# Optimization experiments

Hardware: AMD Instinct MI355X
Metric: run time of the kernel (lower is better)

Reference implementation:

```python
import jax, jax.numpy as jnp
import numpy as np

B, S, NB = 2, 1024, 64
V, D, L, H, F = 1024, 512, 12, 8, 2048
DH = D // H
MAX_BARS = 256


def _ln(x, g, b):
    m = x.mean(-1, keepdims=True)
    v = ((x - m) ** 2).mean(-1, keepdims=True)
    return (x - m) * jax.lax.rsqrt(v + 1e-5) * g + b


def _rope(x, pos):
    # x: (B, T, H, DH), pos: (T,)
    half = x.shape[-1] // 2
    inv = 10000.0 ** (-jnp.arange(half, dtype=jnp.float32) / half)
    f = pos.astype(jnp.float32)[:, None] * inv  # (T, half)
    cos = jnp.cos(f)[None, :, None, :]
    sin = jnp.sin(f)[None, :, None, :]
    x1, x2 = x[..., :half], x[..., half:]
    return jnp.concatenate([x1 * cos - x2 * sin, x1 * sin + x2 * cos], -1)


def _swiglu(h, w1, w3, w2):
    return (jax.nn.silu(h @ w1) * (h @ w3)) @ w2


def _attention(sum_x, x, Wq, Wk, Wv, Wo, smask, umask, pos_s, pos_r):
    # shared QKV/O projections over both streams; 4-way block mask via concat keys
    b, nb, _ = sum_x.shape
    s = x.shape[1]

    def proj(t, W):
        return (t @ W).reshape(t.shape[0], t.shape[1], H, DH)

    qs = _rope(proj(sum_x, Wq), pos_s)
    qr = _rope(proj(x, Wq), pos_r)
    k = jnp.concatenate([_rope(proj(sum_x, Wk), pos_s), _rope(proj(x, Wk), pos_r)], 1)
    v = jnp.concatenate([proj(sum_x, Wv), proj(x, Wv)], 1)
    scale = DH ** -0.5

    def attend(q, mask):
        sc = jnp.einsum('bqhd,bkhd->bhqk', q, k) * scale
        sc = jnp.where(mask[:, None], sc, -1e9)
        p = jax.nn.softmax(sc, axis=-1)
        o = jnp.einsum('bhqk,bkhd->bqhd', p, v)
        return o.reshape(q.shape[0], q.shape[1], D)

    return attend(qs, smask) @ Wo, attend(qr, umask) @ Wo


def _forward(tok_emb, inst_emb, bar_emb,
             ln_as_g, ln_as_b, ln_ar_g, ln_ar_b,
             ln_fs_g, ln_fs_b, ln_fr_g, ln_fr_b,
             Wq, Wk, Wv, Wo,
             fs_w1, fs_w3, fs_w2, fr_w1, fr_w3, fr_w2,
             out_g, out_b,
             token_ids, chord_ids, instrument_ids, num_bars):
    b, s = token_ids.shape
    nb = num_bars
    x = tok_emb[token_ids] + inst_emb[jnp.clip(instrument_ids, 0, 129)]
    sum_x = jnp.broadcast_to(bar_emb[:nb][None], (b, nb, tok_emb.shape[1]))

    bars = jnp.arange(nb)
    idx = jnp.arange(s)
    # ss: summary b attends summaries b' <= b (causal over bars)
    ss = jnp.broadcast_to(jnp.tril(jnp.ones((nb, nb), bool))[None], (b, nb, nb))
    # sr: summary b summarizes regular tokens in bar b
    sr = chord_ids[:, None, :] == bars[None, :, None]  # (B, nb, S)
    smask = jnp.concatenate([ss, sr], -1)  # (B, nb, nb+S)
    # rs: regular i attends summaries of strictly previous bars
    rs = bars[None, None, :] < chord_ids[:, :, None]  # (B, S, nb)
    # rr: regular i attends regular j in same bar, causally
    rr = (chord_ids[:, :, None] == chord_ids[:, None, :]) & (idx[:, None] >= idx[None, :])
    umask = jnp.concatenate([rs, rr], -1)  # (B, S, nb+S)

    pos_s = jnp.arange(nb)
    pos_r = jnp.arange(s)

    for l in range(Wq.shape[0]):
        a_s, a_r = _attention(_ln(sum_x, ln_as_g[l], ln_as_b[l]),
                              _ln(x, ln_ar_g[l], ln_ar_b[l]),
                              Wq[l], Wk[l], Wv[l], Wo[l], smask, umask, pos_s, pos_r)
        sum_x = sum_x + a_s
        x = x + a_r
        sum_x = sum_x + _swiglu(_ln(sum_x, ln_fs_g[l], ln_fs_b[l]), fs_w1[l], fs_w3[l], fs_w2[l])
        x = x + _swiglu(_ln(x, ln_fr_g[l], ln_fr_b[l]), fr_w1[l], fr_w3[l], fr_w2[l])

    x = _ln(x, out_g, out_b)
    return x @ tok_emb.T  # tied lm_head


def setup_inputs():
    key = jax.random.key(0)
    it = iter(jax.random.split(key, 40))

    def nrm(shape):
        return jax.random.normal(next(it), shape, jnp.float32) * 0.02

    inp = {
        'token_ids': jax.random.randint(next(it), (B, S), 0, V),
        'chord_ids': jnp.sort(jax.random.randint(next(it), (B, S), 0, NB), axis=-1),
        'instrument_ids': jax.random.randint(next(it), (B, S), 0, 130),
        'num_bars': NB,
        'tok_emb': nrm((V, D)),
        'inst_emb': nrm((130, D)),
        'bar_emb': nrm((MAX_BARS, D)),
        'ln_as_g': jnp.ones((L, D)), 'ln_as_b': jnp.zeros((L, D)),
        'ln_ar_g': jnp.ones((L, D)), 'ln_ar_b': jnp.zeros((L, D)),
        'ln_fs_g': jnp.ones((L, D)), 'ln_fs_b': jnp.zeros((L, D)),
        'ln_fr_g': jnp.ones((L, D)), 'ln_fr_b': jnp.zeros((L, D)),
        'Wq': nrm((L, D, D)), 'Wk': nrm((L, D, D)),
        'Wv': nrm((L, D, D)), 'Wo': nrm((L, D, D)),
        'fs_w1': nrm((L, D, F)), 'fs_w3': nrm((L, D, F)), 'fs_w2': nrm((L, F, D)),
        'fr_w1': nrm((L, D, F)), 'fr_w3': nrm((L, D, F)), 'fr_w2': nrm((L, F, D)),
        'out_g': jnp.ones((D,)), 'out_b': jnp.zeros((D,)),
    }
    return inp


def reference(token_ids, chord_ids, instrument_ids, num_bars,
              tok_emb, inst_emb, bar_emb,
              ln_as_g, ln_as_b, ln_ar_g, ln_ar_b,
              ln_fs_g, ln_fs_b, ln_fr_g, ln_fr_b,
              Wq, Wk, Wv, Wo,
              fs_w1, fs_w3, fs_w2, fr_w1, fr_w3, fr_w2,
              out_g, out_b):
    return _forward(tok_emb, inst_emb, bar_emb,
                    ln_as_g, ln_as_b, ln_ar_g, ln_ar_b,
                    ln_fs_g, ln_fs_b, ln_fr_g, ln_fr_b,
                    Wq, Wk, Wv, Wo,
                    fs_w1, fs_w3, fs_w2, fr_w1, fr_w3, fr_w2,
                    out_g, out_b,
                    token_ids, chord_ids, instrument_ids, num_bars)
```

## Files before the change

### kernel.cpp

```cpp
#include <hip/hip_runtime.h>
#include <stdint.h>

#define NB 64
#define BATCH 2
#define SEQ 1024
#define DMODEL 512
#define NHEAD 8
#define DHEAD 64
#define FDIM 2048
#define NLAYER 12
#define VOCAB 1024
#define KTOT (NB + SEQ)
#define RSUM (BATCH * NB)
#define RREG (BATCH * SEQ)
#define RTOT (RSUM + RREG)

using bf16x8 = __attribute__((ext_vector_type(8))) short;
using bf16x4 = __attribute__((ext_vector_type(4))) short;
using f32x4  = __attribute__((ext_vector_type(4))) float;

__device__ __forceinline__ unsigned short f2bf(float f) {
  union { float f; unsigned u; } c; c.f = f;
  return (unsigned short)((c.u + 0x7fffu + ((c.u >> 16) & 1u)) >> 16);
}
__device__ __forceinline__ float bf2f(unsigned short s) {
  union { unsigned u; float f; } c; c.u = ((unsigned)s) << 16;
  return c.f;
}

template<int R>
__device__ __forceinline__ void stage_tile(
    const unsigned short* __restrict__ G, int K, int base_row, int k0,
    unsigned short (*lds)[64], int wid, int lane)
{
  const int rl = lane >> 3;
  const int j  = lane & 7;
  #pragma unroll
  for (int c = 0; c < R / 32; ++c) {
    const int r0 = wid * (R / 4) + c * 8;
    const int row = r0 + rl;
    const unsigned short* g = G + (size_t)(base_row + row) * K + k0
                                + ((j ^ (row & 7)) << 3);
    __builtin_amdgcn_global_load_lds(
        (const __attribute__((address_space(1))) void*)g,
        (__attribute__((address_space(3))) void*)&lds[r0][0], 16, 0, 0);
  }
}

__device__ __forceinline__ bf16x8 lds_frag(const unsigned short (*lds)[64],
                                           int row, int cc) {
  return *(const bf16x8*)&lds[row][(cc ^ (row & 7)) << 3];
}

template<int BM, int BN, int EPI>
__global__ __launch_bounds__(256) void gemm_bt(
    const unsigned short* __restrict__ A, const unsigned short* __restrict__ B0,
    const unsigned short* __restrict__ B1,
    void* __restrict__ Cout, const float* resid, int N, int K,
    const float* __restrict__ cost, const float* __restrict__ sint,
    unsigned short* __restrict__ kcat, unsigned short* __restrict__ vcat)
{
  constexpr int BK = 64;
  constexpr int WM = BM / 2, WN = BN / 2;
  constexpr int FM = WM / 16, FN = WN / 16;
  constexpr int SM_STAGE = (BM + BN) * BK * 2;
  constexpr int SM_CT = (EPI == 3) ? 64 * 66 * 4 : 0;
  constexpr int SMSZ = SM_STAGE > SM_CT ? SM_STAGE : SM_CT;
  __shared__ __align__(16) unsigned char smem[SMSZ];
  auto As = (unsigned short (*)[BK])smem;
  auto Bs = (unsigned short (*)[BK])(smem + BM * BK * 2);
  const int bm = blockIdx.y * BM, bn = blockIdx.x * BN;
  const unsigned short* __restrict__ BT = (bm < RSUM) ? B0 : B1;
  const int tid = threadIdx.x;
  const int wid = tid >> 6, lane = tid & 63;
  const int wm = wid >> 1, wn = wid & 1;
  const int lr = lane & 15, lk = lane >> 4;
  f32x4 acc[FM][FN] = {};
  for (int k0 = 0; k0 < K; k0 += BK) {
    __syncthreads();
    stage_tile<BM>(A,  K, bm, k0, As, wid, lane);
    stage_tile<BN>(BT, K, bn, k0, Bs, wid, lane);
    __syncthreads();
    #pragma unroll
    for (int kk = 0; kk < 2; ++kk) {
      bf16x8 af[FM], bfr[FN];
      #pragma unroll
      for (int m = 0; m < FM; ++m)
        af[m] = lds_frag(As, wm * WM + m * 16 + lr, kk * 4 + lk);
      #pragma unroll
      for (int n = 0; n < FN; ++n)
        bfr[n] = lds_frag(Bs, wn * WN + n * 16 + lr, kk * 4 + lk);
      #pragma unroll
      for (int m = 0; m < FM; ++m)
        #pragma unroll
        for (int n = 0; n < FN; ++n)
          acc[m][n] = __builtin_amdgcn_mfma_f32_16x16x32_bf16(af[m], bfr[n], acc[m][n], 0, 0, 0);
    }
  }
  if constexpr (EPI == 3) {
    __syncthreads();
    auto ct = (float (*)[66])smem;
    #pragma unroll
    for (int m = 0; m < FM; ++m)
      #pragma unroll
      for (int n = 0; n < FN; ++n)
        #pragma unroll
        for (int i = 0; i < 4; ++i)
          ct[wm * WM + m * 16 + lk * 4 + i][wn * WN + n * 16 + lr] = acc[m][n][i];
    __syncthreads();
    const int r = tid >> 2, quad = tid & 3;
    const int tr = bm + r;
    int b, pos, catrow;
    if (tr < RSUM) { b = tr >> 6; pos = tr & (NB - 1); catrow = pos; }
    else { const int rr = tr - RSUM; b = rr >> 10; pos = rr & (SEQ - 1); catrow = NB + pos; }
    const int part = bn >> 9;
    const int head = (bn & 511) >> 6;
    const size_t obase = ((size_t)(b * NHEAD + head) * KTOT + catrow) * DHEAD + quad * 16;
    union { unsigned short u[16]; uint4 q[2]; } ob;
    if (part == 2) {
      #pragma unroll
      for (int j = 0; j < 16; ++j) ob.u[j] = f2bf(ct[r][quad * 16 + j]);
      *(uint4*)&vcat[obase] = ob.q[0];
      *(uint4*)&vcat[obase + 8] = ob.q[1];
    } else {
      #pragma unroll
      for (int j = 0; j < 16; ++j) {
        const int d = quad * 16 + j;
        const float v = ct[r][d];
        const float other = ct[r][d ^ 32];
        const float cs = cost[pos * 32 + (d & 31)];
        const float sn = sint[pos * 32 + (d & 31)];
        ob.u[j] = f2bf((d < 32) ? (v * cs - other * sn) : (other * sn + v * cs));
      }
      unsigned short* dst = part ? kcat : (unsigned short*)Cout;
      *(uint4*)&dst[obase] = ob.q[0];
      *(uint4*)&dst[obase + 8] = ob.q[1];
    }
    return;
  }
  #pragma unroll
  for (int m = 0; m < FM; ++m)
    #pragma unroll
    for (int n = 0; n < FN; ++n)
      #pragma unroll
      for (int i = 0; i < 4; ++i) {
        int row = bm + wm * WM + m * 16 + lk * 4 + i;
        int col = bn + wn * WN + n * 16 + lr;
        float v = acc[m][n][i];
        if constexpr (EPI == 1) {
          const float other = __shfl_xor(v, 1, 64);
          if (!(lr & 1)) {
            const float g = v, u = other;
            const float hv = (g / (1.f + __expf(-g))) * u;
            unsigned short* C = (unsigned short*)Cout;
            C[(size_t)row * (N >> 1) + (col >> 1)] = f2bf(hv);
          }
        } else if constexpr (EPI == 2) {
          unsigned short* C = (unsigned short*)Cout;
          C[(size_t)row * N + col] = f2bf(v);
        } else {
          float* C = (float*)Cout;
          size_t idx = (size_t)row * N + col;
          if (resid) v += resid[idx];
          C[idx] = v;
        }
      }
}

__global__ __launch_bounds__(256) void transpose_conv_kernel(
    const float* __restrict__ src, unsigned short* __restrict__ dst,
    int K, int N, size_t sstride, size_t dstride, int rmul, int radd)
{
  __shared__ float tile[32][33];
  const float* s = src + (size_t)blockIdx.z * sstride;
  unsigned short* d = dst + (size_t)blockIdx.z * dstride;
  const int k0 = blockIdx.y * 32, n0 = blockIdx.x * 32;
  const int tx = threadIdx.x & 31, ty = threadIdx.x >> 5;
  #pragma unroll
  for (int i = 0; i < 32; i += 8)
    tile[ty + i][tx] = s[(size_t)(k0 + ty + i) * N + n0 + tx];
  __syncthreads();
  #pragma unroll
  for (int i = 0; i < 32; i += 8)
    d[((size_t)(n0 + ty + i) * rmul + radd) * K + k0 + tx] = f2bf(tile[tx][ty + i]);
}

__global__ __launch_bounds__(256) void convert_bf16_kernel(
    const float* __restrict__ src, unsigned short* __restrict__ dst)
{
  const int i = (blockIdx.x * 256 + threadIdx.x) * 4;
  const float4 v = *(const float4*)&src[i];
  union { unsigned short u[4]; uint2 q; } o;
  o.u[0] = f2bf(v.x); o.u[1] = f2bf(v.y); o.u[2] = f2bf(v.z); o.u[3] = f2bf(v.w);
  *(uint2*)&dst[i] = o.q;
}

__global__ __launch_bounds__(128) void embed_kernel(
    const int* __restrict__ tok, const int* __restrict__ inst,
    const float* __restrict__ tok_emb, const float* __restrict__ inst_emb,
    const float* __restrict__ bar_emb, float* __restrict__ z)
{
  const int r = blockIdx.x, t = threadIdx.x;
  float4 val;
  if (r < RSUM) {
    const int bar = r & (NB - 1);
    val = *(const float4*)&bar_emb[(size_t)bar * DMODEL + t * 4];
  } else {
    const int rr = r - RSUM;
    const int b = rr >> 10, i = rr & (SEQ - 1);
    const int tk = tok[b * SEQ + i];
    int ins = inst[b * SEQ + i];
    ins = ins < 0 ? 0 : (ins > 129 ? 129 : ins);
    const float4 a = *(const float4*)&tok_emb[(size_t)tk * DMODEL + t * 4];
    const float4 cc = *(const float4*)&inst_emb[(size_t)ins * DMODEL + t * 4];
    val.x = a.x + cc.x; val.y = a.y + cc.y; val.z = a.z + cc.z; val.w = a.w + cc.w;
  }
  *(float4*)&z[(size_t)r * DMODEL + t * 4] = val;
}

__global__ __launch_bounds__(256) void ln_dual_kernel(
    const float* __restrict__ x, const float* __restrict__ g_s,
    const float* __restrict__ b_s, const float* __restrict__ g_r,
    const float* __restrict__ b_r, unsigned short* __restrict__ out)
{
  const int wid = threadIdx.x >> 6, lane = threadIdx.x & 63;
  const size_t row = (size_t)blockIdx.x * 4 + wid;
  const float* g = (row < RSUM) ? g_s : g_r;
  const float* bb = (row < RSUM) ? b_s : b_r;
  const float* xr = x + row * DMODEL + lane * 8;
  float v[8];
  *(float4*)&v[0] = *(const float4*)&xr[0];
  *(float4*)&v[4] = *(const float4*)&xr[4];
  float s = 0.f;
  #pragma unroll
  for (int j = 0; j < 8; ++j) s += v[j];
  #pragma unroll
  for (int o = 32; o > 0; o >>= 1) s += __shfl_xor(s, o, 64);
  const float mean = s * (1.f / DMODEL);
  float vs = 0.f;
  #pragma unroll
  for (int j = 0; j < 8; ++j) { float d = v[j] - mean; vs += d * d; }
  #pragma unroll
  for (int o = 32; o > 0; o >>= 1) vs += __shfl_xor(vs, o, 64);
  const float rs = rsqrtf(vs * (1.f / DMODEL) + 1e-5f);
  float gg[8], bv[8];
  *(float4*)&gg[0] = *(const float4*)&g[lane * 8];
  *(float4*)&gg[4] = *(const float4*)&g[lane * 8 + 4];
  *(float4*)&bv[0] = *(const float4*)&bb[lane * 8];
  *(float4*)&bv[4] = *(const float4*)&bb[lane * 8 + 4];
  union { unsigned short u[8]; uint4 q; } o8;
  #pragma unroll
  for (int j = 0; j < 8; ++j) o8.u[j] = f2bf((v[j] - mean) * rs * gg[j] + bv[j]);
  *(uint4*)&out[row * DMODEL + lane * 8] = o8.q;
}

__global__ __launch_bounds__(256) void ln_kernel(
    const float* __restrict__ x, const float* __restrict__ g,
    const float* __restrict__ bb, unsigned short* __restrict__ out)
{
  const int wid = threadIdx.x >> 6, lane = threadIdx.x & 63;
  const size_t row = (size_t)blockIdx.x * 4 + wid;
  const float* xr = x + row * DMODEL + lane * 8;
  float v[8];
  *(float4*)&v[0] = *(const float4*)&xr[0];
  *(float4*)&v[4] = *(const float4*)&xr[4];
  float s = 0.f;
  #pragma unroll
  for (int j = 0; j < 8; ++j) s += v[j];
  #pragma unroll
  for (int o = 32; o > 0; o >>= 1) s += __shfl_xor(s, o, 64);
  const float mean = s * (1.f / DMODEL);
  float vs = 0.f;
  #pragma unroll
  for (int j = 0; j < 8; ++j) { float d = v[j] - mean; vs += d * d; }
  #pragma unroll
  for (int o = 32; o > 0; o >>= 1) vs += __shfl_xor(vs, o, 64);
  const float rs = rsqrtf(vs * (1.f / DMODEL) + 1e-5f);
  float gg[8], bv[8];
  *(float4*)&gg[0] = *(const float4*)&g[lane * 8];
  *(float4*)&gg[4] = *(const float4*)&g[lane * 8 + 4];
  *(float4*)&bv[0] = *(const float4*)&bb[lane * 8];
  *(float4*)&bv[4] = *(const float4*)&bb[lane * 8 + 4];
  union { unsigned short u[8]; uint4 q; } o8;
  #pragma unroll
  for (int j = 0; j < 8; ++j) o8.u[j] = f2bf((v[j] - mean) * rs * gg[j] + bv[j]);
  *(uint4*)&out[row * DMODEL + lane * 8] = o8.q;
}

__global__ void rope_table_kernel(float* __restrict__ cost, float* __restrict__ sint) {
  const int pos = blockIdx.x, j = threadIdx.x;
  const float inv = powf(10000.f, -(float)j / 32.f);
  const float f = (float)pos * inv;
  cost[pos * 32 + j] = cosf(f);
  sint[pos * 32 + j] = sinf(f);
}

__global__ void segstart_kernel(const int* __restrict__ chord, int* __restrict__ seg) {
  const int b = blockIdx.x, t = threadIdx.x;
  if (t <= NB) {
    int lo = 0, hi = SEQ;
    while (lo < hi) {
      int mid = (lo + hi) >> 1;
      if (chord[b * SEQ + mid] < t) lo = mid + 1; else hi = mid;
    }
    seg[b * (NB + 1) + t] = lo;
  }
}

__global__ __launch_bounds__(256) void attn_kernel(
    const unsigned short* __restrict__ q_cat, const unsigned short* __restrict__ k_cat,
    const unsigned short* __restrict__ v_cat, const int* __restrict__ seg,
    const int* __restrict__ chord, unsigned short* __restrict__ att)
{
  const int h = blockIdx.y, b = blockIdx.z;
  const int wid = threadIdx.x >> 6, lane = threadIdx.x & 63;
  const int qi = blockIdx.x * 4 + wid;
  int qrow, nsum, s0, nk, outrow;
  if (qi < NB) {
    const int c = qi;
    s0 = seg[b * (NB + 1) + c];
    const int s1 = seg[b * (NB + 1) + c + 1];
    qrow = c; nsum = c + 1; nk = nsum + (s1 - s0);
    outrow = b * NB + c;
  } else {
    const int i = qi - NB;
    const int c = chord[b * SEQ + i];
    s0 = seg[b * (NB + 1) + c];
    qrow = NB + i; nsum = c; nk = nsum + (i - s0 + 1);
    outrow = RSUM + b * SEQ + i;
  }
  const size_t bh = (size_t)(b * NHEAD + h) * KTOT * DHEAD;
  const unsigned short* __restrict__ Kp = k_cat + bh;
  const unsigned short* __restrict__ Vp = v_cat + bh;
  __shared__ __align__(16) float qsh[4][DHEAD];
  __shared__ __align__(16) float psh[4][64];
  qsh[wid][lane] = bf2f(q_cat[bh + (size_t)qrow * DHEAD + lane]) * 0.125f;
  const int lq = lane & 3;
  const int lkey = lane >> 2;
  const int kk = lane >> 4;
  const int dd = lane & 15;
  float m = -1e30f, l = 0.f;
  float4 o4 = {0.f, 0.f, 0.f, 0.f};
  for (int t0 = 0; t0 < nk; t0 += 64) {
    float sv[4];
    float tmax = -3.0e38f;
    #pragma unroll
    for (int pass = 0; pass < 4; ++pass) {
      const int t = t0 + pass * 16 + lkey;
      int kr = (t < nsum) ? t : (NB + s0 + (t - nsum));
      if (kr > KTOT - 1) kr = KTOT - 1;
      const bf16x8* krp = (const bf16x8*)(Kp + (size_t)kr * DHEAD + lq * 16);
      const bf16x8 k0v = krp[0], k1v = krp[1];
      float a = 0.f;
      #pragma unroll
      for (int d2 = 0; d2 < 8; ++d2)
        a = fmaf(qsh[wid][lq * 16 + d2], bf2f((unsigned short)k0v[d2]), a);
      #pragma unroll
      for (int d2 = 0; d2 < 8; ++d2)
        a = fmaf(qsh[wid][lq * 16 + 8 + d2], bf2f((unsigned short)k1v[d2]), a);
      a += __shfl_xor(a, 1, 64);
      a += __shfl_xor(a, 2, 64);
      sv[pass] = (t < nk) ? a : -3.0e38f;
      tmax = fmaxf(tmax, sv[pass]);
    }
    #pragma unroll
    for (int off = 32; off > 0; off >>= 1) tmax = fmaxf(tmax, __shfl_xor(tmax, off, 64));
    const float mn = fmaxf(m, tmax);
    float psum = 0.f;
    #pragma unroll
    for (int pass = 0; pass < 4; ++pass) {
      const float pp = __expf(sv[pass] - mn);
      psum += pp;
      if (lq == 0) psh[wid][pass * 16 + lkey] = pp;
    }
    psum *= 0.25f;
    #pragma unroll
    for (int off = 32; off > 0; off >>= 1) psum += __shfl_xor(psum, off, 64);
    const float scale = __expf(m - mn);
    l = l * scale + psum;
    o4.x *= scale; o4.y *= scale; o4.z *= scale; o4.w *= scale;
    m = mn;
    #pragma unroll
    for (int j = 0; j < 16; ++j) {
      const int toff = j * 4 + kk;
      const float p = psh[wid][toff];
      const int tk = t0 + toff;
      int kr = (tk < nsum) ? tk : (NB + s0 + (tk - nsum));
      if (kr > KTOT - 1) kr = KTOT - 1;
      const bf16x4 vv = *(const bf16x4*)&Vp[(size_t)kr * DHEAD + dd * 4];
      o4.x = fmaf(p, bf2f((unsigned short)vv[0]), o4.x);
      o4.y = fmaf(p, bf2f((unsigned short)vv[1]), o4.y);
      o4.z = fmaf(p, bf2f((unsigned short)vv[2]), o4.z);
      o4.w = fmaf(p, bf2f((unsigned short)vv[3]), o4.w);
    }
  }
  #pragma unroll
  for (int off = 16; off <= 32; off <<= 1) {
    o4.x += __shfl_xor(o4.x, off, 64);
    o4.y += __shfl_xor(o4.y, off, 64);
    o4.z += __shfl_xor(o4.z, off, 64);
    o4.w += __shfl_xor(o4.w, off, 64);
  }
  if (kk == 0) {
    const float invl = 1.f / l;
    union { unsigned short u[4]; uint2 q; } ob;
    ob.u[0] = f2bf(o4.x * invl); ob.u[1] = f2bf(o4.y * invl);
    ob.u[2] = f2bf(o4.z * invl); ob.u[3] = f2bf(o4.w * invl);
    *(uint2*)&att[(size_t)outrow * DMODEL + h * DHEAD + dd * 4] = ob.q;
  }
}

extern "C" void kernel_launch(void* const* d_in, const int* in_sizes, int n_in,
                              void* d_out, int out_size, void* d_ws, size_t ws_size,
                              hipStream_t stream)
{
  const int* tok      = (const int*)d_in[0];
  const int* chord    = (const int*)d_in[1];
  const int* inst     = (const int*)d_in[2];
  const float* tok_emb  = (const float*)d_in[4];
  const float* inst_emb = (const float*)d_in[5];
  const float* bar_emb  = (const float*)d_in[6];
  const float* ln_as_g = (const float*)d_in[7];
  const float* ln_as_b = (const float*)d_in[8];
  const float* ln_ar_g = (const float*)d_in[9];
  const float* ln_ar_b = (const float*)d_in[10];
  const float* ln_fs_g = (const float*)d_in[11];
  const float* ln_fs_b = (const float*)d_in[12];
  const float* ln_fr_g = (const float*)d_in[13];
  const float* ln_fr_b = (const float*)d_in[14];
  const float* Wq = (const float*)d_in[15];
  const float* Wk = (const float*)d_in[16];
  const float* Wv = (const float*)d_in[17];
  const float* Wo = (const float*)d_in[18];
  const float* fs_w1 = (const float*)d_in[19];
  const float* fs_w3 = (const float*)d_in[20];
  const float* fs_w2 = (const float*)d_in[21];
  const float* fr_w1 = (const float*)d_in[22];
  const float* fr_w3 = (const float*)d_in[23];
  const float* fr_w2 = (const float*)d_in[24];
  const float* out_g = (const float*)d_in[25];
  const float* out_b = (const float*)d_in[26];

  char* p = (char*)d_ws;
  auto alloc = [&](size_t bytes) -> void* {
    void* r = (void*)p;
    p += (bytes + 255) & ~(size_t)255;
    return r;
  };
  unsigned short* WqkvT  = (unsigned short*)alloc((size_t)NLAYER * 1536 * 512 * 2);
  unsigned short* WoT    = (unsigned short*)alloc((size_t)NLAYER * 512 * 512 * 2);
  unsigned short* fsW13T = (unsigned short*)alloc((size_t)NLAYER * 4096 * 512 * 2);
  unsigned short* frW13T = (unsigned short*)alloc((size_t)NLAYER * 4096 * 512 * 2);
  unsigned short* fsW2T  = (unsigned short*)alloc((size_t)NLAYER * 512 * 2048 * 2);
  unsigned short* frW2T  = (unsigned short*)alloc((size_t)NLAYER * 512 * 2048 * 2);
  unsigned short* tokT   = (unsigned short*)alloc((size_t)VOCAB * DMODEL * 2);
  float* z           = (float*)alloc((size_t)RTOT * DMODEL * 4);
  unsigned short* zn = (unsigned short*)alloc((size_t)RTOT * DMODEL * 2);
  unsigned short* q_cat = (unsigned short*)alloc((size_t)BATCH * NHEAD * KTOT * DHEAD * 2);
  unsigned short* k_cat = (unsigned short*)alloc((size_t)BATCH * NHEAD * KTOT * DHEAD * 2);
  unsigned short* v_cat = (unsigned short*)alloc((size_t)BATCH * NHEAD * KTOT * DHEAD * 2);
  unsigned short* att = (unsigned short*)alloc((size_t)RTOT * DMODEL * 2);
  unsigned short* h1 = (unsigned short*)alloc((size_t)RTOT * FDIM * 2);
  float* cost        = (float*)alloc((size_t)SEQ * 32 * 4);
  float* sint        = (float*)alloc((size_t)SEQ * 32 * 4);
  int* seg           = (int*)alloc((size_t)BATCH * (NB + 1) * 4);
  if ((size_t)(p - (char*)d_ws) > ws_size) return;

  transpose_conv_kernel<<<dim3(16, 16, NLAYER), 256, 0, stream>>>(Wq, WqkvT,                    512, 512,  (size_t)512*512,  (size_t)1536*512, 1, 0);
  transpose_conv_kernel<<<dim3(16, 16, NLAYER), 256, 0, stream>>>(Wk, WqkvT + (size_t)512*512,  512, 512,  (size_t)512*512,  (size_t)1536*512, 1, 0);
  transpose_conv_kernel<<<dim3(16, 16, NLAYER), 256, 0, stream>>>(Wv, WqkvT + (size_t)1024*512, 512, 512,  (size_t)512*512,  (size_t)1536*512, 1, 0);
  transpose_conv_kernel<<<dim3(16, 16, NLAYER), 256, 0, stream>>>(Wo, WoT,                      512, 512,  (size_t)512*512,  (size_t)512*512,  1, 0);
  transpose_conv_kernel<<<dim3(64, 16, NLAYER), 256, 0, stream>>>(fs_w1, fsW13T, 512, 2048, (size_t)512*2048, (size_t)4096*512, 2, 0);
  transpose_conv_kernel<<<dim3(64, 16, NLAYER), 256, 0, stream>>>(fs_w3, fsW13T, 512, 2048, (size_t)512*2048, (size_t)4096*512, 2, 1);
  transpose_conv_kernel<<<dim3(64, 16, NLAYER), 256, 0, stream>>>(fr_w1, frW13T, 512, 2048, (size_t)512*2048, (size_t)4096*512, 2, 0);
  transpose_conv_kernel<<<dim3(64, 16, NLAYER), 256, 0, stream>>>(fr_w3, frW13T, 512, 2048, (size_t)512*2048, (size_t)4096*512, 2, 1);
  transpose_conv_kernel<<<dim3(16, 64, NLAYER), 256, 0, stream>>>(fs_w2, fsW2T, 2048, 512, (size_t)2048*512, (size_t)512*2048, 1, 0);
  transpose_conv_kernel<<<dim3(16, 64, NLAYER), 256, 0, stream>>>(fr_w2, frW2T, 2048, 512, (size_t)2048*512, (size_t)512*2048, 1, 0);
  convert_bf16_kernel<<<VOCAB * DMODEL / 1024, 256, 0, stream>>>(tok_emb, tokT);

  embed_kernel<<<RTOT, 128, 0, stream>>>(tok, inst, tok_emb, inst_emb, bar_emb, z);
  rope_table_kernel<<<SEQ, 32, 0, stream>>>(cost, sint);
  segstart_kernel<<<BATCH, 128, 0, stream>>>(chord, seg);

  for (int l = 0; l < NLAYER; ++l) {
    const size_t ld = (size_t)l * DMODEL;
    ln_dual_kernel<<<RTOT / 4, 256, 0, stream>>>(z, ln_as_g + ld, ln_as_b + ld,
                                                 ln_ar_g + ld, ln_ar_b + ld, zn);
    gemm_bt<64, 64, 3><<<dim3(1536 / 64, RTOT / 64), 256, 0, stream>>>(
        zn, WqkvT + (size_t)l * 1536 * 512, WqkvT + (size_t)l * 1536 * 512,
        q_cat, nullptr, 1536, 512, cost, sint, k_cat, v_cat);
    attn_kernel<<<dim3(KTOT / 4, NHEAD, BATCH), 256, 0, stream>>>(q_cat, k_cat, v_cat, seg, chord, att);
    gemm_bt<64, 32, 0><<<dim3(512 / 32, RTOT / 64), 256, 0, stream>>>(
        att, WoT + (size_t)l * 512 * 512, WoT + (size_t)l * 512 * 512,
        z, z, 512, 512, nullptr, nullptr, nullptr, nullptr);
    ln_dual_kernel<<<RTOT / 4, 256, 0, stream>>>(z, ln_fs_g + ld, ln_fs_b + ld,
                                                 ln_fr_g + ld, ln_fr_b + ld, zn);
    gemm_bt<64, 64, 1><<<dim3(4096 / 64, RTOT / 64), 256, 0, stream>>>(
        zn, fsW13T + (size_t)l * 4096 * 512, frW13T + (size_t)l * 4096 * 512,
        h1, nullptr, 4096, 512, nullptr, nullptr, nullptr, nullptr);
    gemm_bt<64, 32, 0><<<dim3(512 / 32, RTOT / 64), 256, 0, stream>>>(
        h1, fsW2T + (size_t)l * 512 * 2048, frW2T + (size_t)l * 512 * 2048,
        z, z, 512, 2048, nullptr, nullptr, nullptr, nullptr);
  }

  ln_kernel<<<RREG / 4, 256, 0, stream>>>(z + (size_t)RSUM * DMODEL, out_g, out_b,
                                          zn + (size_t)RSUM * DMODEL);
  gemm_bt<64, 64, 0><<<dim3(VOCAB / 64, RREG / 64), 256, 0, stream>>>(
      zn + (size_t)RSUM * DMODEL, tokT, tokT, (float*)d_out, nullptr, VOCAB, 512,
      nullptr, nullptr, nullptr, nullptr);
}
```

Before: 1.320 ms.

## Fuse LayerNorm into GEMM A-tile staging and drop standalone LN kernels

```diff
diff --git a/kernel.cpp b/kernel.cpp
--- a/kernel.cpp
+++ b/kernel.cpp
@@ -52,13 +52,15 @@
   return *(const bf16x8*)&lds[row][(cc ^ (row & 7)) << 3];
 }
 
-template<int BM, int BN, int EPI>
+template<int BM, int BN, int EPI, bool LNF>
 __global__ __launch_bounds__(256) void gemm_bt(
-    const unsigned short* __restrict__ A, const unsigned short* __restrict__ B0,
+    const void* __restrict__ Ap, const unsigned short* __restrict__ B0,
     const unsigned short* __restrict__ B1,
     void* __restrict__ Cout, const float* resid, int N, int K,
     const float* __restrict__ cost, const float* __restrict__ sint,
-    unsigned short* __restrict__ kcat, unsigned short* __restrict__ vcat)
+    unsigned short* __restrict__ kcat, unsigned short* __restrict__ vcat,
+    const float* __restrict__ g_s, const float* __restrict__ b_s,
+    const float* __restrict__ g_r, const float* __restrict__ b_r)
 {
   constexpr int BK = 64;
   constexpr int WM = BM / 2, WN = BN / 2;
@@ -67,6 +69,7 @@
   constexpr int SM_CT = (EPI == 3) ? 64 * 66 * 4 : 0;
   constexpr int SMSZ = SM_STAGE > SM_CT ? SM_STAGE : SM_CT;
   __shared__ __align__(16) unsigned char smem[SMSZ];
+  __shared__ float rstats[BM * 2];
   auto As = (unsigned short (*)[BK])smem;
   auto Bs = (unsigned short (*)[BK])(smem + BM * BK * 2);
   const int bm = blockIdx.y * BM, bn = blockIdx.x * BN;
@@ -75,10 +78,57 @@
   const int wid = tid >> 6, lane = tid & 63;
   const int wm = wid >> 1, wn = wid & 1;
   const int lr = lane & 15, lk = lane >> 4;
+  const float* __restrict__ Az = (const float*)Ap;
+  const unsigned short* __restrict__ Ab = (const unsigned short*)Ap;
+  const float* __restrict__ gsel = (bm < RSUM) ? g_s : g_r;
+  const float* __restrict__ bsel = (bm < RSUM) ? b_s : b_r;
+  if constexpr (LNF) {
+    const int r = tid >> 2, q = tid & 3;
+    const float* src = Az + (size_t)(bm + r) * K + q * 128;
+    float s = 0.f, ss = 0.f;
+    #pragma unroll 8
+    for (int j = 0; j < 32; ++j) {
+      const float4 v = *(const float4*)&src[j * 4];
+      s += v.x + v.y + v.z + v.w;
+      ss += v.x * v.x + v.y * v.y + v.z * v.z + v.w * v.w;
+    }
+    s  += __shfl_xor(s, 1, 64);  s  += __shfl_xor(s, 2, 64);
+    ss += __shfl_xor(ss, 1, 64); ss += __shfl_xor(ss, 2, 64);
+    if (q == 0) {
+      const float mean = s * (1.f / DMODEL);
+      const float var = ss * (1.f / DMODEL) - mean * mean;
+      rstats[r * 2] = mean;
+      rstats[r * 2 + 1] = rsqrtf(fmaxf(var, 0.f) + 1e-5f);
+    }
+  }
   f32x4 acc[FM][FN] = {};
   for (int k0 = 0; k0 < K; k0 += BK) {
     __syncthreads();
-    stage_tile<BM>(A,  K, bm, k0, As, wid, lane);
+    if constexpr (LNF) {
+      const int r = tid >> 2, q = tid & 3;
+      const float mean = rstats[r * 2], rstd = rstats[r * 2 + 1];
+      const float* src = Az + (size_t)(bm + r) * K + k0 + q * 16;
+      const float* gp = gsel + k0 + q * 16;
+      const float* bp = bsel + k0 + q * 16;
+      #pragma unroll
+      for (int c = 0; c < 2; ++c) {
+        float v[8], gv[8], bv[8];
+        *(float4*)&v[0]  = *(const float4*)&src[c * 8];
+        *(float4*)&v[4]  = *(const float4*)&src[c * 8 + 4];
+        *(float4*)&gv[0] = *(const float4*)&gp[c * 8];
+        *(float4*)&gv[4] = *(const float4*)&gp[c * 8 + 4];
+        *(float4*)&bv[0] = *(const float4*)&bp[c * 8];
+        *(float4*)&bv[4] = *(const float4*)&bp[c * 8 + 4];
+        union { unsigned short u[8]; uint4 qd; } ob;
+        #pragma unroll
+        for (int j = 0; j < 8; ++j)
+          ob.u[j] = f2bf((v[j] - mean) * rstd * gv[j] + bv[j]);
+        const int slot = (q * 2 + c) ^ (r & 7);
+        *(uint4*)&As[r][slot * 8] = ob.qd;
+      }
+    } else {
+      stage_tile<BM>(Ab, K, bm, k0, As, wid, lane);
+    }
     stage_tile<BN>(BT, K, bn, k0, Bs, wid, lane);
     __syncthreads();
     #pragma unroll
@@ -216,75 +266,6 @@
     val.x = a.x + cc.x; val.y = a.y + cc.y; val.z = a.z + cc.z; val.w = a.w + cc.w;
   }
   *(float4*)&z[(size_t)r * DMODEL + t * 4] = val;
-}
-
-__global__ __launch_bounds__(256) void ln_dual_kernel(
-    const float* __restrict__ x, const float* __restrict__ g_s,
-    const float* __restrict__ b_s, const float* __restrict__ g_r,
-    const float* __restrict__ b_r, unsigned short* __restrict__ out)
-{
-  const int wid = threadIdx.x >> 6, lane = threadIdx.x & 63;
-  const size_t row = (size_t)blockIdx.x * 4 + wid;
-  const float* g = (row < RSUM) ? g_s : g_r;
-  const float* bb = (row < RSUM) ? b_s : b_r;
-  const float* xr = x + row * DMODEL + lane * 8;
-  float v[8];
-  *(float4*)&v[0] = *(const float4*)&xr[0];
-  *(float4*)&v[4] = *(const float4*)&xr[4];
-  float s = 0.f;
-  #pragma unroll
-  for (int j = 0; j < 8; ++j) s += v[j];
-  #pragma unroll
-  for (int o = 32; o > 0; o >>= 1) s += __shfl_xor(s, o, 64);
-  const float mean = s * (1.f / DMODEL);
-  float vs = 0.f;
-  #pragma unroll
-  for (int j = 0; j < 8; ++j) { float d = v[j] - mean; vs += d * d; }
-  #pragma unroll
-  for (int o = 32; o > 0; o >>= 1) vs += __shfl_xor(vs, o, 64);
-  const float rs = rsqrtf(vs * (1.f / DMODEL) + 1e-5f);
-  float gg[8], bv[8];
-  *(float4*)&gg[0] = *(const float4*)&g[lane * 8];
-  *(float4*)&gg[4] = *(const float4*)&g[lane * 8 + 4];
-  *(float4*)&bv[0] = *(const float4*)&bb[lane * 8];
-  *(float4*)&bv[4] = *(const float4*)&bb[lane * 8 + 4];
-  union { unsigned short u[8]; uint4 q; } o8;
-  #pragma unroll
-  for (int j = 0; j < 8; ++j) o8.u[j] = f2bf((v[j] - mean) * rs * gg[j] + bv[j]);
-  *(uint4*)&out[row * DMODEL + lane * 8] = o8.q;
-}
-
-__global__ __launch_bounds__(256) void ln_kernel(
-    const float* __restrict__ x, const float* __restrict__ g,
-    const float* __restrict__ bb, unsigned short* __restrict__ out)
-{
-  const int wid = threadIdx.x >> 6, lane = threadIdx.x & 63;
-  const size_t row = (size_t)blockIdx.x * 4 + wid;
-  const float* xr = x + row * DMODEL + lane * 8;
-  float v[8];
-  *(float4*)&v[0] = *(const float4*)&xr[0];
-  *(float4*)&v[4] = *(const float4*)&xr[4];
-  float s = 0.f;
-  #pragma unroll
-  for (int j = 0; j < 8; ++j) s += v[j];
-  #pragma unroll
-  for (int o = 32; o > 0; o >>= 1) s += __shfl_xor(s, o, 64);
-  const float mean = s * (1.f / DMODEL);
-  float vs = 0.f;
-  #pragma unroll
-  for (int j = 0; j < 8; ++j) { float d = v[j] - mean; vs += d * d; }
-  #pragma unroll
-  for (int o = 32; o > 0; o >>= 1) vs += __shfl_xor(vs, o, 64);
-  const float rs = rsqrtf(vs * (1.f / DMODEL) + 1e-5f);
-  float gg[8], bv[8];
-  *(float4*)&gg[0] = *(const float4*)&g[lane * 8];
-  *(float4*)&gg[4] = *(const float4*)&g[lane * 8 + 4];
-  *(float4*)&bv[0] = *(const float4*)&bb[lane * 8];
-  *(float4*)&bv[4] = *(const float4*)&bb[lane * 8 + 4];
-  union { unsigned short u[8]; uint4 q; } o8;
-  #pragma unroll
-  for (int j = 0; j < 8; ++j) o8.u[j] = f2bf((v[j] - mean) * rs * gg[j] + bv[j]);
-  *(uint4*)&out[row * DMODEL + lane * 8] = o8.q;
 }
 
 __global__ void rope_table_kernel(float* __restrict__ cost, float* __restrict__ sint) {
@@ -455,7 +436,6 @@
   unsigned short* frW2T  = (unsigned short*)alloc((size_t)NLAYER * 512 * 2048 * 2);
   unsigned short* tokT   = (unsigned short*)alloc((size_t)VOCAB * DMODEL * 2);
   float* z           = (float*)alloc((size_t)RTOT * DMODEL * 4);
-  unsigned short* zn = (unsigned short*)alloc((size_t)RTOT * DMODEL * 2);
   unsigned short* q_cat = (unsigned short*)alloc((size_t)BATCH * NHEAD * KTOT * DHEAD * 2);
   unsigned short* k_cat = (unsigned short*)alloc((size_t)BATCH * NHEAD * KTOT * DHEAD * 2);
   unsigned short* v_cat = (unsigned short*)alloc((size_t)BATCH * NHEAD * KTOT * DHEAD * 2);
@@ -484,28 +464,26 @@
 
   for (int l = 0; l < NLAYER; ++l) {
     const size_t ld = (size_t)l * DMODEL;
-    ln_dual_kernel<<<RTOT / 4, 256, 0, stream>>>(z, ln_as_g + ld, ln_as_b + ld,
-                                                 ln_ar_g + ld, ln_ar_b + ld, zn);
-    gemm_bt<64, 64, 3><<<dim3(1536 / 64, RTOT / 64), 256, 0, stream>>>(
-        zn, WqkvT + (size_t)l * 1536 * 512, WqkvT + (size_t)l * 1536 * 512,
-        q_cat, nullptr, 1536, 512, cost, sint, k_cat, v_cat);
+    gemm_bt<64, 64, 3, true><<<dim3(1536 / 64, RTOT / 64), 256, 0, stream>>>(
+        z, WqkvT + (size_t)l * 1536 * 512, WqkvT + (size_t)l * 1536 * 512,
+        q_cat, nullptr, 1536, 512, cost, sint, k_cat, v_cat,
+        ln_as_g + ld, ln_as_b + ld, ln_ar_g + ld, ln_ar_b + ld);
     attn_kernel<<<dim3(KTOT / 4, NHEAD, BATCH), 256, 0, stream>>>(q_cat, k_cat, v_cat, seg, chord, att);
-    gemm_bt<64, 32, 0><<<dim3(512 / 32, RTOT / 64), 256, 0, stream>>>(
+    gemm_bt<64, 32, 0, false><<<dim3(512 / 32, RTOT / 64), 256, 0, stream>>>(
         att, WoT + (size_t)l * 512 * 512, WoT + (size_t)l * 512 * 512,
-        z, z, 512, 512, nullptr, nullptr, nullptr, nullptr);
-    ln_dual_kernel<<<RTOT / 4, 256, 0, stream>>>(z, ln_fs_g + ld, ln_fs_b + ld,
-                                                 ln_fr_g + ld, ln_fr_b + ld, zn);
-    gemm_bt<64, 64, 1><<<dim3(4096 / 64, RTOT / 64), 256, 0, stream>>>(
-        zn, fsW13T + (size_t)l * 4096 * 512, frW13T + (size_t)l * 4096 * 512,
-        h1, nullptr, 4096, 512, nullptr, nullptr, nullptr, nullptr);
-    gemm_bt<64, 32, 0><<<dim3(512 / 32, RTOT / 64), 256, 0, stream>>>(
+        z, z, 512, 512, nullptr, nullptr, nullptr, nullptr,
+        nullptr, nullptr, nullptr, nullptr);
+    gemm_bt<64, 64, 1, true><<<dim3(4096 / 64, RTOT / 64), 256, 0, stream>>>(
+        z, fsW13T + (size_t)l * 4096 * 512, frW13T + (size_t)l * 4096 * 512,
+        h1, nullptr, 4096, 512, nullptr, nullptr, nullptr, nullptr,
+        ln_fs_g + ld, ln_fs_b + ld, ln_fr_g + ld, ln_fr_b + ld);
+    gemm_bt<64, 32, 0, false><<<dim3(512 / 32, RTOT / 64), 256, 0, stream>>>(
         h1, fsW2T + (size_t)l * 512 * 2048, frW2T + (size_t)l * 512 * 2048,
-        z, z, 512, 2048, nullptr, nullptr, nullptr, nullptr);
-  }
-
-  ln_kernel<<<RREG / 4, 256, 0, stream>>>(z + (size_t)RSUM * DMODEL, out_g, out_b,
-                                          zn + (size_t)RSUM * DMODEL);
-  gemm_bt<64, 64, 0><<<dim3(VOCAB / 64, RREG / 64), 256, 0, stream>>>(
-      zn + (size_t)RSUM * DMODEL, tokT, tokT, (float*)d_out, nullptr, VOCAB, 512,
-      nullptr, nullptr, nullptr, nullptr);
-}
+        z, z, 512, 2048, nullptr, nullptr, nullptr, nullptr,
+        nullptr, nullptr, nullptr, nullptr);
+  }
+
+  gemm_bt<64, 64, 0, true><<<dim3(VOCAB / 64, RREG / 64), 256, 0, stream>>>(
+      z + (size_t)RSUM * DMODEL, tokT, tokT, (float*)d_out, nullptr, VOCAB, 512,
+      nullptr, nullptr, nullptr, nullptr, out_g, out_b, out_g, out_b);
+}
```

Result: slower. 2.521 ms (+91.0%).
